# Optimization experiments

Hardware: AMD Instinct MI355X
Metric: run time of the kernel (lower is better)

## Reference

```python
import jax, jax.numpy as jnp
import numpy as np

NEG_SLOPE = 0.2    # DenseGATConv attention leaky_relu slope (PyG default)
ACT_SLOPE = 0.01   # block activation LeakyReLU slope
HEADS = 3


def setup_inputs() -> dict:
    key = jax.random.key(0)
    B, N, D0, D1, D2, H = 512, 128, 128, 64, 64, HEADS
    ks = jax.random.split(key, 7)
    x = jax.random.normal(ks[0], (B * N, D0), jnp.float32)
    # equal-sized graphs: sorted graph ids, N atoms per graph
    batch_mask = jnp.repeat(jnp.arange(B, dtype=jnp.int32), N)
    s0 = 1.0 / np.sqrt(D0)
    s1 = 1.0 / np.sqrt(D1)
    s2 = 1.0 / np.sqrt(D2)
    W1 = jax.random.normal(ks[1], (D0, H * D1), jnp.float32) * s0
    att_src1 = jax.random.normal(ks[2], (H, D1), jnp.float32) * s1
    att_dst1 = jax.random.normal(ks[3], (H, D1), jnp.float32) * s1
    b1 = jnp.zeros((D1,), jnp.float32)
    W2 = jax.random.normal(ks[4], (D1, H * D2), jnp.float32) * s1
    att_src2 = jax.random.normal(ks[5], (H, D2), jnp.float32) * s2
    att_dst2 = jax.random.normal(ks[6], (H, D2), jnp.float32) * s2
    b2 = jnp.zeros((D2,), jnp.float32)
    return dict(x=x, batch_mask=batch_mask, W1=W1, att_src1=att_src1,
                att_dst1=att_dst1, b1=b1, W2=W2, att_src2=att_src2,
                att_dst2=att_dst2, b2=b2, batch_size=B, n_max=N)


def _dense_gat(x, adj, W, a_src, a_dst, b):
    # x: [B, N, Din], adj: [B, N, N] (self-loops already set). concat=False.
    B, N, _ = x.shape
    H, C = a_src.shape
    h = (x @ W).reshape(B, N, H, C)                       # lin (no bias)
    a_s = jnp.einsum('bnhc,hc->bnh', h, a_src)            # per-node src score
    a_d = jnp.einsum('bnhc,hc->bnh', h, a_dst)            # per-node dst score
    alpha = a_s[:, None, :, :] + a_d[:, :, None, :]       # [B, i, j, H]
    alpha = jax.nn.leaky_relu(alpha, NEG_SLOPE)
    alpha = jnp.where(adj[..., None] == 0, -jnp.inf, alpha)
    alpha = jax.nn.softmax(alpha, axis=2)                 # over source j
    out = jnp.einsum('bijh,bjhc->bihc', alpha, h)         # [B, N, H, C]
    return out.mean(axis=2) + b                           # concat=False -> head mean


def reference(x, batch_mask, W1, att_src1, att_dst1, b1,
              W2, att_src2, att_dst2, b2, batch_size, n_max):
    total, D0 = x.shape
    counts = jnp.bincount(batch_mask, length=batch_size)          # atoms per graph
    starts = jnp.cumsum(counts) - counts
    pos = jnp.arange(total) - starts[batch_mask]                  # slot within graph
    # to_dense_batch
    xd = jnp.zeros((batch_size, n_max, D0), x.dtype).at[batch_mask, pos].set(x)
    node_in = jnp.arange(n_max)[None, :] < counts[:, None]        # [B, N] valid mask
    # block adjacency: fully connected within each graph, diag zeroed...
    adj = (node_in[:, :, None] & node_in[:, None, :]).astype(x.dtype)
    # ...then DenseGATConv add_loop=True re-sets the full diagonal to 1
    adj = jnp.where(jnp.eye(n_max, dtype=bool), jnp.asarray(1.0, x.dtype), adj)
    h = _dense_gat(xd, adj, W1, att_src1, att_dst1, b1)
    h = jax.nn.leaky_relu(h, ACT_SLOPE)
    h = _dense_gat(h, adj, W2, att_src2, att_dst2, b2)
    h = jax.nn.leaky_relu(h, ACT_SLOPE)
    return jnp.sum(h, axis=1)                                     # sum pooling -> [B, D2]
```

## Files before the change

kernel.cpp:

```cpp
#include <hip/hip_runtime.h>
#include <stdint.h>

#define NROW 128

typedef __attribute__((ext_vector_type(8))) __bf16 bf16x8;
typedef __attribute__((ext_vector_type(4))) float  f32x4;

static __device__ __forceinline__ uint16_t f2bf(float f) {
    union { float f; uint32_t i; } v; v.f = f;
    uint32_t x = v.i;
    return (uint16_t)((x + 0x7FFFu + ((x >> 16) & 1u)) >> 16);
}
static __device__ __forceinline__ uint16_t bfbits(float f) {
    __bf16 h = (__bf16)f;
    union { __bf16 h; uint16_t u; } c; c.h = h; return c.u;
}
static __device__ __forceinline__ float fexp2(float x) {
#if __has_builtin(__builtin_amdgcn_exp2f)
    return __builtin_amdgcn_exp2f(x);
#else
    return exp2f(x);
#endif
}
static __device__ __forceinline__ float frcp(float x) {
#if __has_builtin(__builtin_amdgcn_rcpf)
    return __builtin_amdgcn_rcpf(x);
#else
    return 1.0f / x;
#endif
}

__global__ __launch_bounds__(256)
void prep_kernel(const float* __restrict__ W1, const float* __restrict__ as1,
                 const float* __restrict__ ad1,
                 const float* __restrict__ W2, const float* __restrict__ as2,
                 const float* __restrict__ ad2,
                 uint16_t* __restrict__ wT1x, uint16_t* __restrict__ wT2x)
{
    constexpr float LOG2E = 1.4426950408889634f;
    int bid = blockIdx.x, t = threadIdx.x;
    if (bid < 96) {
        int idx = bid * 256 + t;
        int c = idx >> 7, k = idx & 127;
        wT1x[c * 128 + k] = f2bf(W1[k * 192 + c]);
    } else if (bid < 144) {
        int idx = (bid - 96) * 256 + t;
        int c = idx >> 6, k = idx & 63;
        wT2x[c * 64 + k] = f2bf(W2[k * 192 + c]);
    } else if (bid == 144) {
#pragma unroll
        for (int e = 0; e < 3; ++e) {
            int idx = t + e * 256;
            if (idx < 768) {
                int j = idx >> 7, k = idx & 127, hd = j >> 1;
                const float* av = (j & 1) ? ad1 : as1;
                float s = 0.f;
                for (int c = 0; c < 64; ++c)
                    s += W1[k * 192 + hd * 64 + c] * av[hd * 64 + c];
                wT1x[(192 + j) * 128 + k] = f2bf(s * LOG2E);
            }
        }
#pragma unroll
        for (int e = 0; e < 5; ++e) {
            int idx = t + e * 256;
            if (idx < 1280) wT1x[198 * 128 + idx] = 0;
        }
    } else {
#pragma unroll
        for (int e = 0; e < 2; ++e) {
            int idx = t + e * 256;
            if (idx < 384) {
                int j = idx >> 6, k = idx & 63, hd = j >> 1;
                const float* av = (j & 1) ? ad2 : as2;
                float s = 0.f;
                for (int c = 0; c < 64; ++c)
                    s += W2[k * 192 + hd * 64 + c] * av[hd * 64 + c];
                wT2x[(192 + j) * 64 + k] = f2bf(s * LOG2E);
            }
        }
#pragma unroll
        for (int e = 0; e < 3; ++e) {
            int idx = t + e * 256;
            if (idx < 640) wT2x[198 * 64 + idx] = 0;
        }
    }
}

static __device__ __forceinline__ uint32_t hT_off(int row, int colbytes) {
    uint32_t bo = (uint32_t)(row * 256 + colbytes);
    return bo ^ (uint32_t)((row & 7) << 4);
}
#define S2 72

static __device__ __forceinline__
void scores_and_hT(const f32x4* hacc, uint16_t* hT, float* as_s, float* ad_s,
                   int i0, int lr, int lg)
{
    if (lr < 6) {
        float* dst = (lr & 1) ? ad_s : as_s;
        int hd = lr >> 1;
#pragma unroll
        for (int r = 0; r < 4; ++r)
            dst[hd * 128 + i0 + lg * 4 + r] = hacc[12][r];
    }
#pragma unroll
    for (int f = 0; f < 12; ++f) {
        uint32_t p0 = (uint32_t)bfbits(hacc[f][0]) | ((uint32_t)bfbits(hacc[f][1]) << 16);
        uint32_t p1 = (uint32_t)bfbits(hacc[f][2]) | ((uint32_t)bfbits(hacc[f][3]) << 16);
        *(uint2*)((char*)hT + hT_off(f * 16 + lr, (i0 + lg * 4) * 2)) = make_uint2(p0, p1);
    }
}

static __device__ __forceinline__
void softmax_pv(const uint16_t* hT, const float* as_s, const float* ad_s,
                f32x4* oacc, int i0, int lr, int lg)
{
#pragma unroll
    for (int f = 0; f < 4; ++f) oacc[f] = (f32x4){0.f, 0.f, 0.f, 0.f};

#pragma unroll
    for (int hd = 0; hd < 3; ++hd) {
        float ad  = ad_s[hd * 128 + i0 + lr];
        float adm = ad - 16.0f;
        float adn = 0.2f * ad - 16.0f;
        float zp = 0.f;
        f32x4 tacc[4];
#pragma unroll
        for (int f = 0; f < 4; ++f) tacc[f] = (f32x4){0.f, 0.f, 0.f, 0.f};
#pragma unroll
        for (int q = 0; q < 4; ++q) {
            float4 s0 = *(const float4*)&as_s[hd * 128 + q * 32 + lg * 8];
            float4 s1 = *(const float4*)&as_s[hd * 128 + q * 32 + lg * 8 + 4];
            float sv[8] = {s0.x, s0.y, s0.z, s0.w, s1.x, s1.y, s1.z, s1.w};
            bf16x8 apq;
#pragma unroll
            for (int m = 0; m < 8; ++m) {
                float ev = fexp2(fmaxf(sv[m] + adm, __builtin_fmaf(sv[m], 0.2f, adn)));
                zp += ev;
                apq[m] = (__bf16)ev;
            }
#pragma unroll
            for (int f = 0; f < 4; ++f) {
                bf16x8 bfv = *(const bf16x8*)((const char*)hT +
                                 hT_off(hd * 64 + f * 16 + lr, q * 64 + lg * 16));
                tacc[f] = __builtin_amdgcn_mfma_f32_16x16x32_bf16(apq, bfv, tacc[f], 0, 0, 0);
            }
        }
        zp += __shfl_xor(zp, 16);
        zp += __shfl_xor(zp, 32);
        float inv = frcp(3.0f * zp);
        float invr[4];
#pragma unroll
        for (int r = 0; r < 4; ++r) invr[r] = __shfl(inv, lg * 4 + r);
#pragma unroll
        for (int f = 0; f < 4; ++f)
#pragma unroll
            for (int r = 0; r < 4; ++r) oacc[f][r] += tacc[f][r] * invr[r];
    }
}

__global__ __launch_bounds__(512, 4)
void fused_kernel(const float* __restrict__ x,
                  const uint16_t* __restrict__ wT1g, const uint16_t* __restrict__ wT2g,
                  const float* __restrict__ b1g, const float* __restrict__ b2g,
                  float* __restrict__ outp)
{
    __shared__ __align__(16) char smem[53248];
    __shared__ __align__(16) float as_s[3 * 128];
    __shared__ __align__(16) float ad_s[3 * 128];
    __shared__ float bia[128];
    __shared__ float pool_s[8 * 64];

    uint16_t* x2T  = (uint16_t*)smem;
    uint16_t* wT2l = (uint16_t*)(smem + 128 * S2 * 2);

    const int b = blockIdx.x, t = threadIdx.x;
    const int w = t >> 6, lr = t & 15, lg = (t >> 4) & 3;
    const int i0 = w * 16;

    bf16x8 afr[4];
    {
        const float* xg = x + ((long)b * NROW + i0 + lr) * 128;
        float4 r0[4], r1[4];
#pragma unroll
        for (int q = 0; q < 4; ++q) {
            r0[q] = *(const float4*)(xg + q * 32 + lg * 8);
            r1[q] = *(const float4*)(xg + q * 32 + lg * 8 + 4);
        }
#pragma unroll
        for (int q = 0; q < 4; ++q) {
            bf16x8 a;
            a[0] = (__bf16)r0[q].x; a[1] = (__bf16)r0[q].y;
            a[2] = (__bf16)r0[q].z; a[3] = (__bf16)r0[q].w;
            a[4] = (__bf16)r1[q].x; a[5] = (__bf16)r1[q].y;
            a[6] = (__bf16)r1[q].z; a[7] = (__bf16)r1[q].w;
            afr[q] = a;
        }
    }
#pragma unroll
    for (int p = 0; p < 7; ++p) {
        int idx = t + p * 512;
        if (idx < 3328) {
            int row = idx >> 4, cb = (idx & 15) * 16;
            *(uint4*)(smem + hT_off(row, cb)) = *(const uint4*)(wT1g + row * 128 + cb / 2);
        }
    }
    if (t < 64) bia[t] = b1g[t];
    else if (t < 128) bia[t] = b2g[t - 64];
    __syncthreads();

    f32x4 hacc[13];
#pragma unroll
    for (int f = 0; f < 13; ++f) hacc[f] = (f32x4){0.f, 0.f, 0.f, 0.f};
#pragma unroll
    for (int q = 0; q < 4; ++q)
#pragma unroll
        for (int f = 0; f < 13; ++f) {
            bf16x8 bfv = *(const bf16x8*)(smem + hT_off(f * 16 + lr, q * 64 + lg * 16));
            hacc[f] = __builtin_amdgcn_mfma_f32_16x16x32_bf16(afr[q], bfv, hacc[f], 0, 0, 0);
        }
    __syncthreads();

    scores_and_hT(hacc, (uint16_t*)smem, as_s, ad_s, i0, lr, lg);
    __syncthreads();

    f32x4 oacc[4];
    softmax_pv((const uint16_t*)smem, as_s, ad_s, oacc, i0, lr, lg);
    __syncthreads();

    {
        uint4 wpre[4];
#pragma unroll
        for (int p = 0; p < 3; ++p) {
            int idx = t + p * 512; int row = idx >> 3; int c8 = (idx & 7) * 8;
            wpre[p] = *(const uint4*)(wT2g + row * 64 + c8);
        }
        if (t < 128) {
            int idx = t + 1536; int row = idx >> 3; int c8 = (idx & 7) * 8;
            wpre[3] = *(const uint4*)(wT2g + row * 64 + c8);
        }
#pragma unroll
        for (int f = 0; f < 4; ++f) {
            int c = f * 16 + lr;
            float bv = bia[c];
#pragma unroll
            for (int r = 0; r < 4; ++r) {
                float v = oacc[f][r] + bv;
                v = fmaxf(v, 0.01f * v);
                x2T[(i0 + lg * 4 + r) * S2 + c] = bfbits(v);
            }
        }
#pragma unroll
        for (int p = 0; p < 3; ++p) {
            int idx = t + p * 512; int row = idx >> 3; int c8 = (idx & 7) * 8;
            *(uint4*)&wT2l[row * S2 + c8] = wpre[p];
        }
        if (t < 128) {
            int idx = t + 1536; int row = idx >> 3; int c8 = (idx & 7) * 8;
            *(uint4*)&wT2l[row * S2 + c8] = wpre[3];
        }
    }
    __syncthreads();

    bf16x8 af2[2];
#pragma unroll
    for (int q = 0; q < 2; ++q)
        af2[q] = *(const bf16x8*)&x2T[(i0 + lr) * S2 + q * 32 + lg * 8];
#pragma unroll
    for (int f = 0; f < 13; ++f) hacc[f] = (f32x4){0.f, 0.f, 0.f, 0.f};
#pragma unroll
    for (int q = 0; q < 2; ++q)
#pragma unroll
        for (int f = 0; f < 13; ++f) {
            bf16x8 bfv = *(const bf16x8*)&wT2l[(f * 16 + lr) * S2 + q * 32 + lg * 8];
            hacc[f] = __builtin_amdgcn_mfma_f32_16x16x32_bf16(af2[q], bfv, hacc[f], 0, 0, 0);
        }
    __syncthreads();

    scores_and_hT(hacc, (uint16_t*)smem, as_s, ad_s, i0, lr, lg);
    __syncthreads();

    softmax_pv((const uint16_t*)smem, as_s, ad_s, oacc, i0, lr, lg);

#pragma unroll
    for (int f = 0; f < 4; ++f) {
        int c = f * 16 + lr;
        float bv = bia[64 + c];
        float s = 0.f;
#pragma unroll
        for (int r = 0; r < 4; ++r) {
            float v = oacc[f][r] + bv;
            v = fmaxf(v, 0.01f * v);
            s += v;
        }
        s += __shfl_xor(s, 16);
        s += __shfl_xor(s, 32);
        if (lg == 0) pool_s[w * 64 + c] = s;
    }
    __syncthreads();
    if (t < 64) {
        float s = 0.f;
#pragma unroll
        for (int q = 0; q < 8; ++q) s += pool_s[q * 64 + t];
        outp[(long)b * 64 + t] = s;
    }
}

extern "C" void kernel_launch(void* const* d_in, const int* in_sizes, int n_in,
                              void* d_out, int out_size, void* d_ws, size_t ws_size,
                              hipStream_t stream)
{
    const float* x   = (const float*)d_in[0];
    const float* W1  = (const float*)d_in[2];
    const float* as1 = (const float*)d_in[3];
    const float* ad1 = (const float*)d_in[4];
    const float* b1  = (const float*)d_in[5];
    const float* W2  = (const float*)d_in[6];
    const float* as2 = (const float*)d_in[7];
    const float* ad2 = (const float*)d_in[8];
    const float* b2  = (const float*)d_in[9];

    uint16_t* wT1x = (uint16_t*)d_ws;
    uint16_t* wT2x = wT1x + 208 * 128;

    prep_kernel<<<146, 256, 0, stream>>>(W1, as1, ad1, W2, as2, ad2, wT1x, wT2x);
    fused_kernel<<<512, 512, 0, stream>>>(x, wT1x, wT2x, b1, b2, (float*)d_out);
}
```

Baseline: 130.4 us.

## Software-pipeline softmax exp with PV MFMAs and spread prep score work across blocks

Softmax-PV now computes the exp block for the next 32-column chunk while issuing the MFMAs for the previous one, double-buffering the bf16 operand and raising wave priority around the MFMAs. The aim is to hide transcendental latency behind matrix work. The second-layer A-fragment loads move ahead of the block barrier, since each wave reads only rows it wrote, guarded by an lgkmcnt wait. The prep kernel splits the attention-projection dot products and zero-fill over 12 blocks instead of 2, shortening that kernel's serial tail. The cost is higher register pressure from the extra live operands.

```diff
diff --git a/kernel.cpp b/kernel.cpp
--- a/kernel.cpp
+++ b/kernel.cpp
@@ -47,41 +47,29 @@
         int idx = (bid - 96) * 256 + t;
         int c = idx >> 6, k = idx & 63;
         wT2x[c * 64 + k] = f2bf(W2[k * 192 + c]);
-    } else if (bid == 144) {
-#pragma unroll
-        for (int e = 0; e < 3; ++e) {
-            int idx = t + e * 256;
-            if (idx < 768) {
-                int j = idx >> 7, k = idx & 127, hd = j >> 1;
-                const float* av = (j & 1) ? ad1 : as1;
-                float s = 0.f;
-                for (int c = 0; c < 64; ++c)
-                    s += W1[k * 192 + hd * 64 + c] * av[hd * 64 + c];
-                wT1x[(192 + j) * 128 + k] = f2bf(s * LOG2E);
-            }
-        }
-#pragma unroll
-        for (int e = 0; e < 5; ++e) {
-            int idx = t + e * 256;
-            if (idx < 1280) wT1x[198 * 128 + idx] = 0;
-        }
     } else {
-#pragma unroll
-        for (int e = 0; e < 2; ++e) {
-            int idx = t + e * 256;
-            if (idx < 384) {
-                int j = idx >> 6, k = idx & 63, hd = j >> 1;
-                const float* av = (j & 1) ? ad2 : as2;
-                float s = 0.f;
-                for (int c = 0; c < 64; ++c)
-                    s += W2[k * 192 + hd * 64 + c] * av[hd * 64 + c];
-                wT2x[(192 + j) * 64 + k] = f2bf(s * LOG2E);
-            }
-        }
-#pragma unroll
-        for (int e = 0; e < 3; ++e) {
-            int idx = t + e * 256;
-            if (idx < 640) wT2x[198 * 64 + idx] = 0;
+        int idx = (bid - 144) * 256 + t;
+        if (idx < 768) {
+            int j = idx >> 7, k = idx & 127, hd = j >> 1;
+            const float* av = (j & 1) ? ad1 : as1;
+            float s = 0.f;
+#pragma unroll 8
+            for (int c = 0; c < 64; ++c)
+                s += W1[k * 192 + hd * 64 + c] * av[hd * 64 + c];
+            wT1x[(192 + j) * 128 + k] = f2bf(s * LOG2E);
+        } else if (idx < 1152) {
+            int i2 = idx - 768;
+            int j = i2 >> 6, k = i2 & 63, hd = j >> 1;
+            const float* av = (j & 1) ? ad2 : as2;
+            float s = 0.f;
+#pragma unroll 8
+            for (int c = 0; c < 64; ++c)
+                s += W2[k * 192 + hd * 64 + c] * av[hd * 64 + c];
+            wT2x[(192 + j) * 64 + k] = f2bf(s * LOG2E);
+        } else if (idx < 2432) {
+            wT1x[198 * 128 + (idx - 1152)] = 0;
+        } else {
+            wT2x[198 * 64 + (idx - 2432)] = 0;
         }
     }
 }
@@ -110,6 +98,30 @@
         *(uint2*)((char*)hT + hT_off(f * 16 + lr, (i0 + lg * 4) * 2)) = make_uint2(p0, p1);
     }
 }
+
+#define EXP_BLOCK(qq, apx) do {                                               \
+    float4 _s0 = *(const float4*)&as_s[hd * 128 + (qq) * 32 + lg * 8];        \
+    float4 _s1 = *(const float4*)&as_s[hd * 128 + (qq) * 32 + lg * 8 + 4];    \
+    float _sv[8] = {_s0.x,_s0.y,_s0.z,_s0.w,_s1.x,_s1.y,_s1.z,_s1.w};         \
+    _Pragma("unroll")                                                         \
+    for (int m = 0; m < 8; ++m) {                                             \
+        float _ev = fexp2(fmaxf(_sv[m] + adm,                                 \
+                                __builtin_fmaf(_sv[m], 0.2f, adn)));          \
+        zp += _ev; apx[m] = (__bf16)_ev;                                      \
+    }                                                                         \
+} while (0)
+
+#define PV_MFMA4(qq, apx) do {                                                \
+    __builtin_amdgcn_s_setprio(1);                                            \
+    _Pragma("unroll")                                                         \
+    for (int f = 0; f < 4; ++f) {                                             \
+        bf16x8 _bfv = *(const bf16x8*)((const char*)hT +                      \
+                         hT_off(hd * 64 + f * 16 + lr, (qq) * 64 + lg * 16)); \
+        tacc[f] = __builtin_amdgcn_mfma_f32_16x16x32_bf16(apx, _bfv,          \
+                                                          tacc[f], 0, 0, 0);  \
+    }                                                                         \
+    __builtin_amdgcn_s_setprio(0);                                            \
+} while (0)
 
 static __device__ __forceinline__
 void softmax_pv(const uint16_t* hT, const float* as_s, const float* ad_s,
@@ -127,25 +139,14 @@
         f32x4 tacc[4];
 #pragma unroll
         for (int f = 0; f < 4; ++f) tacc[f] = (f32x4){0.f, 0.f, 0.f, 0.f};
-#pragma unroll
-        for (int q = 0; q < 4; ++q) {
-            float4 s0 = *(const float4*)&as_s[hd * 128 + q * 32 + lg * 8];
-            float4 s1 = *(const float4*)&as_s[hd * 128 + q * 32 + lg * 8 + 4];
-            float sv[8] = {s0.x, s0.y, s0.z, s0.w, s1.x, s1.y, s1.z, s1.w};
-            bf16x8 apq;
-#pragma unroll
-            for (int m = 0; m < 8; ++m) {
-                float ev = fexp2(fmaxf(sv[m] + adm, __builtin_fmaf(sv[m], 0.2f, adn)));
-                zp += ev;
-                apq[m] = (__bf16)ev;
-            }
-#pragma unroll
-            for (int f = 0; f < 4; ++f) {
-                bf16x8 bfv = *(const bf16x8*)((const char*)hT +
-                                 hT_off(hd * 64 + f * 16 + lr, q * 64 + lg * 16));
-                tacc[f] = __builtin_amdgcn_mfma_f32_16x16x32_bf16(apq, bfv, tacc[f], 0, 0, 0);
-            }
-        }
+
+        bf16x8 apA, apB;
+        EXP_BLOCK(0, apA);
+        EXP_BLOCK(1, apB); PV_MFMA4(0, apA);
+        EXP_BLOCK(2, apA); PV_MFMA4(1, apB);
+        EXP_BLOCK(3, apB); PV_MFMA4(2, apA);
+        PV_MFMA4(3, apB);
+
         zp += __shfl_xor(zp, 16);
         zp += __shfl_xor(zp, 32);
         float inv = frcp(3.0f * zp);
@@ -228,6 +229,7 @@
     softmax_pv((const uint16_t*)smem, as_s, ad_s, oacc, i0, lr, lg);
     __syncthreads();
 
+    bf16x8 af2[2];
     {
         uint4 wpre[4];
 #pragma unroll
@@ -250,6 +252,11 @@
                 x2T[(i0 + lg * 4 + r) * S2 + c] = bfbits(v);
             }
         }
+        asm volatile("s_waitcnt lgkmcnt(0)" ::: "memory");
+        __builtin_amdgcn_sched_barrier(0);
+#pragma unroll
+        for (int q = 0; q < 2; ++q)
+            af2[q] = *(const bf16x8*)&x2T[(i0 + lr) * S2 + q * 32 + lg * 8];
 #pragma unroll
         for (int p = 0; p < 3; ++p) {
             int idx = t + p * 512; int row = idx >> 3; int c8 = (idx & 7) * 8;
@@ -262,10 +269,6 @@
     }
     __syncthreads();
 
-    bf16x8 af2[2];
-#pragma unroll
-    for (int q = 0; q < 2; ++q)
-        af2[q] = *(const bf16x8*)&x2T[(i0 + lr) * S2 + q * 32 + lg * 8];
 #pragma unroll
     for (int f = 0; f < 13; ++f) hacc[f] = (f32x4){0.f, 0.f, 0.f, 0.f};
 #pragma unroll
@@ -323,6 +326,6 @@
     uint16_t* wT1x = (uint16_t*)d_ws;
     uint16_t* wT2x = wT1x + 208 * 128;
 
-    prep_kernel<<<146, 256, 0, stream>>>(W1, as1, ad1, W2, as2, ad2, wT1x, wT2x);
+    prep_kernel<<<156, 256, 0, stream>>>(W1, as1, ad1, W2, as2, ad2, wT1x, wT2x);
     fused_kernel<<<512, 512, 0, stream>>>(x, wT1x, wT2x, b1, b2, (float*)d_out);
 }
```

Measured after the change: 128.1 us. No clear change (-1.8%).
